# Performance work log

Measured on AMD Instinct MI355X. Metric: run time of the kernel, lower is better.

## Reference

```python
import jax, jax.numpy as jnp
import numpy as np

GRID = 8
S = GRID * GRID          # 64 tokens
D = 256                  # embed dim
H = 4                    # heads
HD = D // H              # 64 head dim
L = 8                    # depth
EPS = 1.1920929e-07      # torch.finfo(float32).eps (nn.RMSNorm eps=None)
RADIUS = 2.5


def _grid_coords():
    y, x = np.meshgrid(np.arange(GRID), np.arange(GRID), indexing='ij')
    return np.stack([y.ravel(), x.ravel()], axis=1).astype(np.float32)  # [S,2]


def _rope_cos_sin():
    coords = _grid_coords()
    dim_half = HD // 2  # 32
    inv_freq = 1.0 / (10000.0 ** (np.arange(0, dim_half, 2, dtype=np.float32) / dim_half))  # [16]
    fy = coords[:, 0:1] * inv_freq[None, :]   # [S,16]
    fx = coords[:, 1:2] * inv_freq[None, :]   # [S,16]
    freqs = np.concatenate([fy, fx], axis=-1)  # [S,32]
    emb = np.concatenate([freqs, freqs], axis=-1)  # [S,64]
    return jnp.asarray(np.cos(emb)), jnp.asarray(np.sin(emb))


def _local_mask():
    coords = _grid_coords()
    d = np.sqrt(((coords[:, None, :] - coords[None, :, :]) ** 2).sum(-1))
    return jnp.asarray(d < RADIUS)  # [S,S] bool


COS, SIN = _rope_cos_sin()
MASK_LOCAL = _local_mask()
MASK_GLOBAL = jnp.ones((S, S), dtype=bool)


def rms(x):
    return x * jax.lax.rsqrt(jnp.mean(x * x, axis=-1, keepdims=True) + EPS)


def householder_Q(vs):
    # vs: [R, HD]; Q = prod of reflections applied as in the torch loop
    def step(Q, v):
        vn = jnp.sum(v * v) + 1e-08
        return Q - (2.0 / vn) * jnp.outer(v, v @ Q), None
    Q, _ = jax.lax.scan(step, jnp.eye(HD, dtype=vs.dtype), vs)
    return Q


def rotate_half(x):
    x1, x2 = jnp.split(x, 2, axis=-1)
    return jnp.concatenate([-x2, x1], axis=-1)


def block(x, vs_l, wqkv, wout, wg, bg, wmg, bmg, wmo, bmo, mask):
    B = x.shape[0]
    xn = rms(x)
    qkv = xn @ wqkv                                # [B,S,3D]
    q, k, v = jnp.split(qkv, 3, axis=-1)
    q = q.reshape(B, S, H, HD).transpose(0, 2, 1, 3)   # [B,H,S,HD]
    k = k.reshape(B, S, H, HD).transpose(0, 2, 1, 3)
    v = v.reshape(B, S, H, HD).transpose(0, 2, 1, 3)
    Q = householder_Q(vs_l)                        # [HD,HD]
    # inverse rotation, standard RoPE, forward rotation
    q = q @ Q.T
    k = k @ Q.T
    cos = COS[None, None]                          # [1,1,S,HD]
    sin = SIN[None, None]
    q = q * cos + rotate_half(q) * sin
    k = k * cos + rotate_half(k) * sin
    q = q @ Q
    k = k @ Q
    scores = jnp.einsum('bhqd,bhkd->bhqk', q, k) / jnp.sqrt(jnp.float32(HD))
    scores = jnp.where(mask[None, None], scores, -jnp.inf)
    attn = jax.nn.softmax(scores, axis=-1)
    out = jnp.einsum('bhqk,bhkd->bhqd', attn, v)   # [B,H,S,HD]
    out = out.transpose(0, 2, 1, 3).reshape(B, S, D)
    out = out @ wout
    gate = jax.nn.sigmoid(out @ wg + bg)
    x = x + out * gate
    xn = rms(x)
    m = xn @ wmg + bmg                             # [B,S,8D]
    g, val = jnp.split(m, 2, axis=-1)
    x = x + (val * jax.nn.gelu(g, approximate=False)) @ wmo + bmo
    return x


def setup_inputs() -> dict:
    key = jax.random.key(0)
    ks = jax.random.split(key, 20)
    B = 1024
    s = 0.02
    return {
        'z_t': jax.random.normal(ks[0], (B, 3, 16, 16), jnp.float32),
        'logsnr': jax.random.normal(ks[1], (B,), jnp.float32),
        'w_patch_in': jax.random.normal(ks[2], (20, D), jnp.float32) * s,
        'b_patch_in': jnp.zeros((D,), jnp.float32),
        'vs': jax.random.normal(ks[3], (L, HD // 2, HD), jnp.float32) * s,
        'w_qkv': jax.random.normal(ks[4], (L, D, 3 * D), jnp.float32) * s,
        'w_out': jax.random.normal(ks[5], (L, D, D), jnp.float32) * s,
        'w_gate': jax.random.normal(ks[6], (L, D, D), jnp.float32) * s,
        'b_gate': jnp.zeros((L, D), jnp.float32),
        'w_mlp_gate': jax.random.normal(ks[7], (L, D, 8 * D), jnp.float32) * s,
        'b_mlp_gate': jnp.zeros((L, 8 * D), jnp.float32),
        'w_mlp_out': jax.random.normal(ks[8], (L, 4 * D, D), jnp.float32) * s,
        'b_mlp_out': jnp.zeros((L, D), jnp.float32),
        'norm_final_w': jnp.ones((D,), jnp.float32),
        'w_head': jax.random.normal(ks[9], (D, D), jnp.float32) * s,
        'b_head': jnp.zeros((D,), jnp.float32),
        'w_patch_out': jax.random.normal(ks[10], (D, 12), jnp.float32) * s,
        'b_patch_out': jnp.zeros((12,), jnp.float32),
    }


def reference(z_t, logsnr, w_patch_in, b_patch_in, vs, w_qkv, w_out, w_gate, b_gate,
              w_mlp_gate, b_mlp_gate, w_mlp_out, b_mlp_out, norm_final_w,
              w_head, b_head, w_patch_out, b_patch_out):
    B = z_t.shape[0]
    # patchify: [B,3,16,16] -> [B,64,12] (2x2 patches over 8x8 grid)
    patches = z_t.reshape(B, 3, GRID, 2, GRID, 2).transpose(0, 2, 4, 1, 3, 5).reshape(B, S, 12)
    # Fourier features of logsnr: num_bands=4, max_range=40
    freqs = (2.0 * np.pi / 40.0) * (2.0 ** jnp.arange(4, dtype=jnp.float32))
    args = logsnr[:, None] * freqs                 # [B,4]
    spins = jnp.concatenate([jnp.sin(args), jnp.cos(args)], axis=-1)  # [B,8]
    spins = jnp.broadcast_to(spins[:, None, :], (B, S, 8))
    x = jnp.concatenate([patches, spins], axis=-1) @ w_patch_in + b_patch_in  # [B,S,D]
    for i in range(L):
        mask = MASK_GLOBAL if (i + 1) % 4 == 0 else MASK_LOCAL
        x = block(x, vs[i], w_qkv[i], w_out[i], w_gate[i], b_gate[i],
                  w_mlp_gate[i], b_mlp_gate[i], w_mlp_out[i], b_mlp_out[i], mask)
    x = rms(x) * norm_final_w
    out = x @ w_head + b_head
    z = out @ w_patch_out + b_patch_out            # [B,S,12]
    z = z.reshape(B, GRID, GRID, 3, 2, 2).transpose(0, 3, 1, 4, 2, 5).reshape(B, 3, 16, 16)
    return z
```

## Files before the change

kernel.cpp:

```cpp
#include <hip/hip_runtime.h>

#define DEV static __device__ __forceinline__

typedef float f32x4 __attribute__((ext_vector_type(4)));
typedef short s16x8 __attribute__((ext_vector_type(8)));
typedef __bf16 bf16x8 __attribute__((ext_vector_type(8)));

DEV unsigned short f2bf(float f) {
  union { float f; unsigned u; } v; v.f = f;
  unsigned r = v.u + 0x7FFFu + ((v.u >> 16) & 1u);
  return (unsigned short)(r >> 16);
}
DEV float bf2f(unsigned short h) {
  union { unsigned u; float f; } v; v.u = ((unsigned)h) << 16;
  return v.f;
}
DEV void g2l16(const void* g, void* l) {
  __builtin_amdgcn_global_load_lds((const __attribute__((address_space(1))) void*)g,
                                   (__attribute__((address_space(3))) void*)l, 16, 0, 0);
}
DEV f32x4 mfma16(bf16x8 a, bf16x8 b, f32x4 c) {
  return __builtin_amdgcn_mfma_f32_16x16x32_bf16(a, b, c, 0, 0, 0);
}
DEV int xcd_swz(int bid, int nwg) {
  return (bid & 7) * (nwg >> 3) + (bid >> 3);
}
DEV float gelu_t(float g) {
  float y = 0.7978845608028654f * (g + 0.044715f * g * g * g);
  float th = 1.f - 2.f * __builtin_amdgcn_rcpf(1.f + __expf(2.f * y));
  return 0.5f * g * (1.f + th);
}

__global__ void k_house(const float* __restrict__ VS, float* __restrict__ Qg) {
  const int l = blockIdx.x, t = threadIdx.x;
  float Qc[64];
#pragma unroll
  for (int i = 0; i < 64; i++) Qc[i] = (i == t) ? 1.f : 0.f;
  for (int rr = 0; rr < 32; rr++) {
    float vt = VS[(size_t)l * 2048 + rr * 64 + t];
    float vn = vt * vt;
#pragma unroll
    for (int o = 1; o < 64; o <<= 1) vn += __shfl_xor(vn, o, 64);
    float vv[64];
#pragma unroll
    for (int i = 0; i < 64; i++) vv[i] = __shfl(vt, i, 64);
    float w0 = 0.f, w1 = 0.f, w2 = 0.f, w3 = 0.f;
#pragma unroll
    for (int i = 0; i < 64; i += 4) {
      w0 = fmaf(vv[i + 0], Qc[i + 0], w0);
      w1 = fmaf(vv[i + 1], Qc[i + 1], w1);
      w2 = fmaf(vv[i + 2], Qc[i + 2], w2);
      w3 = fmaf(vv[i + 3], Qc[i + 3], w3);
    }
    float c = (2.f / (vn + 1e-8f)) * ((w0 + w1) + (w2 + w3));
#pragma unroll
    for (int i = 0; i < 64; i++) Qc[i] = fmaf(-vv[i], c, Qc[i]);
  }
#pragma unroll
  for (int i = 0; i < 64; i++) Qg[(size_t)l * 4096 + i * 64 + t] = Qc[i];
}

__global__ void k_rope(float* __restrict__ C, float* __restrict__ Sn) {
  int idx = blockIdx.x * 256 + threadIdx.x;
  if (idx >= 4096) return;
  int s = idx >> 6, d = idx & 63;
  int dh = d & 31;
  float coord = (dh < 16) ? (float)(s >> 3) : (float)(s & 7);
  int fi = dh & 15;
  float invf = powf(10000.f, -(float)fi / 16.f);
  float ang = coord * invf;
  C[idx] = cosf(ang);
  Sn[idx] = sinf(ang);
}

__global__ __launch_bounds__(256) void k_fold_qkv(const float* __restrict__ W,
                                                  const float* __restrict__ Qg,
                                                  unsigned short* __restrict__ out) {
  __shared__ float qrows[16 * 64];
  __shared__ float tr[16 * 256];
  const int l = blockIdx.x / 48, ng = blockIdx.x % 48;
  const int n0 = ng * 16, t = threadIdx.x;
  const float* Wl = W + (size_t)l * 256 * 768;
  float res[16];
  if (n0 < 512) {
    int part = n0 >> 8, h = (n0 & 255) >> 6, j0 = n0 & 63;
    for (int i = t; i < 1024; i += 256) {
      int jj = i >> 6, dd = i & 63;
      qrows[i] = Qg[(size_t)l * 4096 + (j0 + jj) * 64 + dd];
    }
    __syncthreads();
    const float* wrow = Wl + (size_t)t * 768 + part * 256 + h * 64;
    float wreg[64];
    for (int d = 0; d < 64; d++) wreg[d] = wrow[d];
    for (int jj = 0; jj < 16; jj++) {
      float a = 0.f;
      for (int d = 0; d < 64; d++) a += wreg[d] * qrows[jj * 64 + d];
      res[jj] = a;
    }
  } else {
    for (int jj = 0; jj < 16; jj++) res[jj] = Wl[(size_t)t * 768 + n0 + jj];
    __syncthreads();
  }
  __syncthreads();
  for (int jj = 0; jj < 16; jj++) tr[jj * 256 + t] = res[jj];
  __syncthreads();
  size_t base = (size_t)l * 196608 + (size_t)(n0 >> 4) * 4096;
  int kb = t >> 3, jn0 = (t & 7) * 2;
  s16x8 w0, w1;
  for (int u = 0; u < 8; u++) w0[u] = (short)f2bf(tr[jn0 * 256 + kb * 8 + u]);
  for (int u = 0; u < 8; u++) w1[u] = (short)f2bf(tr[(jn0 + 1) * 256 + kb * 8 + u]);
  *(s16x8*)(out + base + (size_t)t * 16) = w0;
  *(s16x8*)(out + base + (size_t)t * 16 + 8) = w1;
}

__global__ __launch_bounds__(256) void k_fold_w2(const float* __restrict__ WO,
                                                 const float* __restrict__ WG,
                                                 unsigned short* __restrict__ out) {
  __shared__ float wgs[256 * 16];
  __shared__ float tr[16 * 256];
  const int l = blockIdx.x >> 5, ng = blockIdx.x & 31;
  const int n0 = ng * 16, t = threadIdx.x;
  const float* WOl = WO + (size_t)l * 65536;
  float res[16];
  if (n0 < 256) {
    for (int jj = 0; jj < 16; jj++) res[jj] = WOl[(size_t)t * 256 + n0 + jj];
  } else {
    int c0 = n0 - 256;
    const float* WGl = WG + (size_t)l * 65536;
    for (int i = t; i < 4096; i += 256) {
      int k = i >> 4, c = i & 15;
      wgs[i] = WGl[(size_t)k * 256 + c0 + c];
    }
    __syncthreads();
    float a[16];
    for (int c = 0; c < 16; c++) a[c] = 0.f;
    for (int k = 0; k < 256; k++) {
      float wo = WOl[(size_t)t * 256 + k];
      for (int c = 0; c < 16; c++) a[c] += wo * wgs[k * 16 + c];
    }
    for (int c = 0; c < 16; c++) res[c] = a[c];
  }
  __syncthreads();
  for (int jj = 0; jj < 16; jj++) tr[jj * 256 + t] = res[jj];
  __syncthreads();
  size_t base = (size_t)l * 131072 + (size_t)(n0 >> 4) * 4096;
  int kb = t >> 3, jn0 = (t & 7) * 2;
  s16x8 w0, w1;
  for (int u = 0; u < 8; u++) w0[u] = (short)f2bf(tr[jn0 * 256 + kb * 8 + u]);
  for (int u = 0; u < 8; u++) w1[u] = (short)f2bf(tr[(jn0 + 1) * 256 + kb * 8 + u]);
  *(s16x8*)(out + base + (size_t)t * 16) = w0;
  *(s16x8*)(out + base + (size_t)t * 16 + 8) = w1;
}

__global__ __launch_bounds__(256) void k_conv_wmg(const float* __restrict__ W,
                                                  unsigned short* __restrict__ out) {
  __shared__ float tr[16 * 256];
  const int l = blockIdx.x >> 7, ng = blockIdx.x & 127;
  const int n0 = ng * 16, t = threadIdx.x;
  const float* src = W + (size_t)l * 256 * 2048 + (size_t)t * 2048 + n0;
  for (int j = 0; j < 16; j++) tr[j * 256 + t] = src[j];
  __syncthreads();
  size_t base = (size_t)l * 524288 + (size_t)ng * 4096;
  int kb = t >> 3, jn0 = (t & 7) * 2;
  s16x8 w0, w1;
  for (int u = 0; u < 8; u++) w0[u] = (short)f2bf(tr[jn0 * 256 + kb * 8 + u]);
  for (int u = 0; u < 8; u++) w1[u] = (short)f2bf(tr[(jn0 + 1) * 256 + kb * 8 + u]);
  *(s16x8*)(out + base + (size_t)t * 16) = w0;
  *(s16x8*)(out + base + (size_t)t * 16 + 8) = w1;
}

__global__ __launch_bounds__(256) void k_conv_wmo(const float* __restrict__ W,
                                                  unsigned short* __restrict__ out) {
  __shared__ float tr[16 * 256];
  const int l = blockIdx.x >> 4, ng = blockIdx.x & 15;
  const int n0 = ng * 16, t = threadIdx.x;
  const float* Wl = W + (size_t)l * 1024 * 256;
  size_t base = (size_t)l * 262144 + (size_t)ng * 16384;
  for (int c4 = 0; c4 < 4; c4++) {
    int k0 = c4 * 256;
    for (int j = 0; j < 16; j++) tr[j * 256 + t] = Wl[(size_t)(k0 + t) * 256 + n0 + j];
    __syncthreads();
    int kb = t >> 3, jn0 = (t & 7) * 2;
    s16x8 w0, w1;
    for (int u = 0; u < 8; u++) w0[u] = (short)f2bf(tr[jn0 * 256 + kb * 8 + u]);
    for (int u = 0; u < 8; u++) w1[u] = (short)f2bf(tr[(jn0 + 1) * 256 + kb * 8 + u]);
    *(s16x8*)(out + base + (size_t)(k0 >> 3) * 128 + (size_t)t * 16) = w0;
    *(s16x8*)(out + base + (size_t)(k0 >> 3) * 128 + (size_t)t * 16 + 8) = w1;
    __syncthreads();
  }
}

__global__ __launch_bounds__(256) void k_fold_head(const float* __restrict__ WH,
                                                   const float* __restrict__ BH,
                                                   const float* __restrict__ WPO,
                                                   const float* __restrict__ BPO,
                                                   float* __restrict__ WHP,
                                                   float* __restrict__ BHP) {
  __shared__ float wpos[256 * 12];
  const int t = threadIdx.x;
  for (int i = t; i < 3072; i += 256) wpos[i] = WPO[i];
  __syncthreads();
  float a[12];
  for (int c = 0; c < 12; c++) a[c] = 0.f;
  const float* whrow = WH + (size_t)t * 256;
  for (int k = 0; k < 256; k++) {
    float w = whrow[k];
    for (int c = 0; c < 12; c++) a[c] += w * wpos[k * 12 + c];
  }
  for (int c = 0; c < 12; c++) WHP[t * 12 + c] = a[c];
  if (t < 12) {
    float b = BPO[t];
    for (int k = 0; k < 256; k++) b += BH[k] * wpos[k * 12 + t];
    BHP[t] = b;
  }
}

__global__ __launch_bounds__(256) void k_embed(const float* __restrict__ ZT,
                                               const float* __restrict__ LOGSNR,
                                               const float* __restrict__ WPI,
                                               const float* __restrict__ BPI,
                                               float* __restrict__ X) {
  __shared__ float zb[768];
  __shared__ float sp[8];
  const int b = blockIdx.x, t = threadIdx.x;
  for (int i = t; i < 768; i += 256) zb[i] = ZT[(size_t)b * 768 + i];
  if (t < 8) {
    float freq = 0.15707963267948966f * (float)(1 << (t & 3));
    float a = LOGSNR[b] * freq;
    sp[t] = (t < 4) ? sinf(a) : cosf(a);
  }
  __syncthreads();
  float wc[20];
  for (int j = 0; j < 20; j++) wc[j] = WPI[j * 256 + t];
  float bk = BPI[t];
  for (int s = 0; s < 64; s++) {
    int gy = s >> 3, gx = s & 7;
    float acc = bk;
    for (int j = 0; j < 12; j++) {
      int cch = j >> 2, py = (j >> 1) & 1, px = j & 1;
      acc += zb[cch * 256 + (gy * 2 + py) * 16 + gx * 2 + px] * wc[j];
    }
    for (int j = 0; j < 8; j++) acc += sp[j] * wc[12 + j];
    X[((size_t)b * 64 + s) * 256 + t] = acc;
  }
}

__global__ __launch_bounds__(256) void k_rms(const float* __restrict__ X,
                                             unsigned short* __restrict__ XN) {
  const int m0 = blockIdx.x * 16, t = threadIdx.x;
  const int r = t >> 4, cj = t & 15;
  const float* row = X + (size_t)(m0 + r) * 256 + cj * 16;
  float4 a = *(const float4*)(row);
  float4 b = *(const float4*)(row + 4);
  float4 c = *(const float4*)(row + 8);
  float4 d = *(const float4*)(row + 12);
  float ss = a.x * a.x + a.y * a.y + a.z * a.z + a.w * a.w +
             b.x * b.x + b.y * b.y + b.z * b.z + b.w * b.w +
             c.x * c.x + c.y * c.y + c.z * c.z + c.w * c.w +
             d.x * d.x + d.y * d.y + d.z * d.z + d.w * d.w;
  for (int o = 1; o < 16; o <<= 1) ss += __shfl_xor(ss, o, 64);
  float rq = rsqrtf(ss * (1.f / 256.f) + 1.1920929e-07f);
  s16x8 v0, v1;
  v0[0] = (short)f2bf(a.x * rq); v0[1] = (short)f2bf(a.y * rq);
  v0[2] = (short)f2bf(a.z * rq); v0[3] = (short)f2bf(a.w * rq);
  v0[4] = (short)f2bf(b.x * rq); v0[5] = (short)f2bf(b.y * rq);
  v0[6] = (short)f2bf(b.z * rq); v0[7] = (short)f2bf(b.w * rq);
  v1[0] = (short)f2bf(c.x * rq); v1[1] = (short)f2bf(c.y * rq);
  v1[2] = (short)f2bf(c.z * rq); v1[3] = (short)f2bf(c.w * rq);
  v1[4] = (short)f2bf(d.x * rq); v1[5] = (short)f2bf(d.y * rq);
  v1[6] = (short)f2bf(d.z * rq); v1[7] = (short)f2bf(d.w * rq);
  size_t base = ((size_t)blockIdx.x * 32 + cj * 2) * 128 + r * 8;
  *(s16x8*)(XN + base) = v0;
  *(s16x8*)(XN + base + 128) = v1;
}

template <int KD, int NT, int MODE>
__global__ __launch_bounds__(256) void k_gemm_single(const unsigned short* __restrict__ A,
                                                     const unsigned short* __restrict__ Bw,
                                                     unsigned short* __restrict__ Cout,
                                                     const float* __restrict__ bias,
                                                     float* __restrict__ X) {
  __shared__ unsigned short sm[17408];
  unsigned short* la = sm;
  unsigned short* lb = sm + 4096;
  const int t = threadIdx.x;
  const int lane = t & 63, wv = t >> 6;
  const int swz = xcd_swz(blockIdx.x, gridDim.x);
  const int bm = swz / NT, bn = swz % NT;
  const int m0 = bm * 128, n0 = bn * 128;
  const int wm = wv >> 1, wn = wv & 1;
  constexpr int KB8 = KD >> 3;

  f32x4 acc[4][4];
  f32x4 zz = {0.f, 0.f, 0.f, 0.f};
  for (int i = 0; i < 4; i++)
    for (int j = 0; j < 4; j++) acc[i][j] = zz;

  for (int k0 = 0; k0 < KD; k0 += 32) {
    const int kb0 = k0 >> 3;
    for (int ii = 0; ii < 2; ii++) {
      size_t mg = (size_t)(m0 >> 4) + ii * 4 + wv;
      g2l16(A + (mg * KB8 + kb0) * 128 + lane * 8, la + (ii * 4 + wv) * 512 + lane * 8);
    }
    for (int ii = 0; ii < 2; ii++) {
      size_t ng = (size_t)(n0 >> 4) + ii * 4 + wv;
      g2l16(Bw + (ng * KB8 + kb0) * 128 + lane * 8, lb + (ii * 4 + wv) * 512 + lane * 8);
    }
    __syncthreads();
    bf16x8 af[4], bb[4];
    for (int i = 0; i < 4; i++) af[i] = *(const bf16x8*)(la + (wm * 4 + i) * 512 + lane * 8);
    for (int j = 0; j < 4; j++) bb[j] = *(const bf16x8*)(lb + (wn * 4 + j) * 512 + lane * 8);
    for (int i = 0; i < 4; i++)
      for (int j = 0; j < 4; j++) acc[i][j] = mfma16(af[i], bb[j], acc[i][j]);
    __syncthreads();
  }

  const int lr = lane & 15, lg = lane >> 4;
  if constexpr (MODE == 0) {
    unsigned short* lc = sm;
    for (int i = 0; i < 4; i++)
      for (int j = 0; j < 4; j++)
        for (int e = 0; e < 4; e++) {
          int r = wm * 64 + i * 16 + lg * 4 + e;
          int c = wn * 64 + j * 16 + lr;
          lc[r * 136 + c] = f2bf(acc[i][j][e]);
        }
    __syncthreads();
    for (int p = 0; p < 8; p++) {
      int r = p * 16 + (t >> 4);
      int c = (t & 15) * 8;
      *(s16x8*)(Cout + (size_t)(m0 + r) * (NT * 128) + n0 + c) = *(const s16x8*)(lc + r * 136 + c);
    }
  } else {
    float* lcf = (float*)sm;
    for (int p = 0; p < 2; p++) {
      if (wm == p) {
        for (int i = 0; i < 4; i++)
          for (int j = 0; j < 4; j++) {
            int c = wn * 64 + j * 16 + lr;
            float bv = bias[n0 + c];
            for (int e = 0; e < 4; e++) {
              int rr = i * 16 + lg * 4 + e;
              lcf[rr * 132 + c] = acc[i][j][e] + bv;
            }
          }
      }
      __syncthreads();
      for (int k = 0; k < 8; k++) {
        int q = t + 256 * k;
        int row = q >> 5, col4 = q & 31;
        float* xp = X + (size_t)(m0 + p * 64 + row) * 256 + n0 + col4 * 4;
        float4 xv = *(float4*)xp;
        const float* lp = lcf + row * 132 + col4 * 4;
        xv.x += lp[0]; xv.y += lp[1]; xv.z += lp[2]; xv.w += lp[3];
        *(float4*)xp = xv;
      }
      __syncthreads();
    }
  }
}

template <int KD, int MODE>
__global__ __launch_bounds__(256) void k_gemm_dual(const unsigned short* __restrict__ A,
                                                   const unsigned short* __restrict__ B0,
                                                   const unsigned short* __restrict__ B1,
                                                   const float* __restrict__ bias,
                                                   float* __restrict__ X,
                                                   unsigned short* __restrict__ Hout,
                                                   int NT) {
  constexpr int SMSH = (MODE == 0) ? 17408 : 16384;
  __shared__ unsigned short sm[SMSH];
  unsigned short* la = sm;
  unsigned short* lb0 = sm + 8192;
  unsigned short* lb1 = sm + 12288;
  const int t = threadIdx.x, lane = t & 63, wv = t >> 6;
  const int swz = xcd_swz(blockIdx.x, gridDim.x);
  const int bm = swz / NT, bn = swz % NT;
  const int m0 = bm * 128, n0 = bn * 64;
  constexpr int KB8 = KD >> 3;
  f32x4 acc0[2][4], acc1[2][4];
  f32x4 zz = {0.f, 0.f, 0.f, 0.f};
  for (int i = 0; i < 2; i++)
    for (int j = 0; j < 4; j++) { acc0[i][j] = zz; acc1[i][j] = zz; }

  for (int k0 = 0; k0 < KD; k0 += 64) {
    const int kb0 = k0 >> 3;
#pragma unroll
    for (int ii = 0; ii < 4; ii++) {
      int task = ii * 4 + wv;
      int mg = task >> 1, g = task & 1;
      g2l16(A + ((size_t)((m0 >> 4) + mg) * KB8 + kb0 + g * 4) * 128 + lane * 8,
            la + task * 512 + lane * 8);
    }
#pragma unroll
    for (int ii = 0; ii < 2; ii++) {
      int task = ii * 4 + wv;
      int ng = task >> 1, g = task & 1;
      size_t srcoff = ((size_t)((n0 >> 4) + ng) * KB8 + kb0 + g * 4) * 128 + lane * 8;
      g2l16(B0 + srcoff, lb0 + task * 512 + lane * 8);
      g2l16(B1 + srcoff, lb1 + task * 512 + lane * 8);
    }
    __syncthreads();
#pragma unroll
    for (int kk = 0; kk < 2; kk++) {
      bf16x8 af[2];
#pragma unroll
      for (int i = 0; i < 2; i++)
        af[i] = *(const bf16x8*)(la + ((wv * 2 + i) * 8 + kk * 4) * 128 + lane * 8);
#pragma unroll
      for (int j = 0; j < 4; j++) {
        bf16x8 b0 = *(const bf16x8*)(lb0 + (j * 8 + kk * 4) * 128 + lane * 8);
        bf16x8 b1 = *(const bf16x8*)(lb1 + (j * 8 + kk * 4) * 128 + lane * 8);
#pragma unroll
        for (int i = 0; i < 2; i++) {
          acc0[i][j] = mfma16(af[i], b0, acc0[i][j]);
          acc1[i][j] = mfma16(af[i], b1, acc1[i][j]);
        }
      }
    }
    __syncthreads();
  }

  const int lr = lane & 15, lg = lane >> 4;
  if constexpr (MODE == 0) {
    float* lcf = (float*)sm;
    for (int i = 0; i < 2; i++)
      for (int j = 0; j < 4; j++) {
        int c = j * 16 + lr;
        float bv = bias[n0 + c];
        for (int e = 0; e < 4; e++) {
          int r = wv * 32 + i * 16 + lg * 4 + e;
          float o = acc0[i][j][e];
          float g = acc1[i][j][e] + bv;
          lcf[r * 68 + c] = o * __builtin_amdgcn_rcpf(1.f + __expf(-g));
        }
      }
    __syncthreads();
    for (int k = 0; k < 8; k++) {
      int q = t + 256 * k;
      int row = q >> 4, col4 = q & 15;
      float* xp = X + (size_t)(m0 + row) * 256 + n0 + col4 * 4;
      float4 xv = *(float4*)xp;
      const float* lp = lcf + row * 68 + col4 * 4;
      xv.x += lp[0]; xv.y += lp[1]; xv.z += lp[2]; xv.w += lp[3];
      *(float4*)xp = xv;
    }
  } else {
    unsigned short* lc = sm;
    for (int i = 0; i < 2; i++)
      for (int j = 0; j < 4; j++) {
        int cl = j * 16 + lr;
        float bg_ = bias[n0 + cl];
        float bv_ = bias[1024 + n0 + cl];
        for (int e = 0; e < 4; e++) {
          int rl = wv * 32 + i * 16 + lg * 4 + e;
          float g = acc0[i][j][e] + bg_;
          float vv = acc1[i][j][e] + bv_;
          lc[rl * 72 + cl] = f2bf(vv * gelu_t(g));
        }
      }
    __syncthreads();
    for (int it = 0; it < 4; it++) {
      int idx = it * 2048 + t * 8;
      int mg_l = idx >> 10, rem = idx & 1023;
      int kb_l = rem >> 7, r = (rem >> 3) & 15;
      *(s16x8*)(Hout + ((size_t)((m0 >> 4) + mg_l) * 128 + (n0 >> 3) + kb_l) * 128 + r * 8) =
          *(const s16x8*)(lc + (mg_l * 16 + r) * 72 + kb_l * 8);
    }
  }
}

__global__ __launch_bounds__(256) void k_attn(const unsigned short* __restrict__ QKV,
                                              const float* __restrict__ CT,
                                              const float* __restrict__ ST,
                                              unsigned short* __restrict__ AO,
                                              int use_local) {
  __shared__ unsigned short sm[16384];
  unsigned short* qs = sm;
  unsigned short* ks = sm + 4096;
  unsigned short* vt = sm + 8192;
  unsigned short* ps = sm + 12288;
  const int blk = blockIdx.x;
  const int b = blk >> 2, h = blk & 3;
  const int t = threadIdx.x, lane = t & 63, wv = t >> 6;
  const size_t rowbase = (size_t)b * 64 * 768;

  {
    int s = t >> 2, dq = (t & 3) * 8;
    const unsigned short* qrow = QKV + rowbase + (size_t)s * 768 + h * 64;
    s16x8 qlo = *(const s16x8*)(qrow + dq);
    s16x8 qhi = *(const s16x8*)(qrow + dq + 32);
    s16x8 klo = *(const s16x8*)(qrow + 256 + dq);
    s16x8 khi = *(const s16x8*)(qrow + 256 + dq + 32);
    s16x8 oql, oqh, okl, okh;
    for (int e = 0; e < 8; e++) {
      float cl = CT[s * 64 + dq + e], sl = ST[s * 64 + dq + e];
      float ch = CT[s * 64 + dq + 32 + e], sh = ST[s * 64 + dq + 32 + e];
      float ql = bf2f((unsigned short)qlo[e]), qh = bf2f((unsigned short)qhi[e]);
      oql[e] = (short)f2bf((ql * cl - qh * sl) * 0.125f);
      oqh[e] = (short)f2bf((qh * ch + ql * sh) * 0.125f);
      float kl = bf2f((unsigned short)klo[e]), kh = bf2f((unsigned short)khi[e]);
      okl[e] = (short)f2bf(kl * cl - kh * sl);
      okh[e] = (short)f2bf(kh * ch + kl * sh);
    }
    int off_lo = (((s >> 4) * 8 + (dq >> 3)) * 16 + (s & 15)) * 8;
    int off_hi = (((s >> 4) * 8 + (dq >> 3) + 4) * 16 + (s & 15)) * 8;
    *(s16x8*)(qs + off_lo) = oql;
    *(s16x8*)(qs + off_hi) = oqh;
    *(s16x8*)(ks + off_lo) = okl;
    *(s16x8*)(ks + off_hi) = okh;
    int d0 = (t & 3) * 16;
    s16x8 v0 = *(const s16x8*)(qrow + 512 + d0);
    s16x8 v1 = *(const s16x8*)(qrow + 512 + d0 + 8);
    for (int e = 0; e < 8; e++) {
      int d = d0 + e;
      vt[(((d >> 4) * 8 + (s >> 3)) * 16 + (d & 15)) * 8 + (s & 7)] = (unsigned short)v0[e];
      d = d0 + 8 + e;
      vt[(((d >> 4) * 8 + (s >> 3)) * 16 + (d & 15)) * 8 + (s & 7)] = (unsigned short)v1[e];
    }
  }
  __syncthreads();

  f32x4 sc[4];
  f32x4 zz = {0.f, 0.f, 0.f, 0.f};
  for (int j = 0; j < 4; j++) sc[j] = zz;
  for (int kk = 0; kk < 2; kk++) {
    bf16x8 aq = *(const bf16x8*)(qs + wv * 1024 + kk * 512 + lane * 8);
    for (int j = 0; j < 4; j++)
      sc[j] = mfma16(aq, *(const bf16x8*)(ks + j * 1024 + kk * 512 + lane * 8), sc[j]);
  }

  const int lr = lane & 15, lg = lane >> 4;
  for (int e = 0; e < 4; e++) {
    int sq = wv * 16 + lg * 4 + e;
    int yq = sq >> 3, xq = sq & 7;
    float mx = -1e30f;
    float vals[4];
    for (int j = 0; j < 4; j++) {
      int sk = j * 16 + lr;
      float v = sc[j][e];
      if (use_local) {
        int dy = yq - (sk >> 3), dx = xq - (sk & 7);
        if (dy * dy + dx * dx > 6) v = -1e30f;
      }
      vals[j] = v;
      mx = fmaxf(mx, v);
    }
    for (int o = 1; o < 16; o <<= 1) mx = fmaxf(mx, __shfl_xor(mx, o, 64));
    float sum = 0.f;
    for (int j = 0; j < 4; j++) {
      float p = __expf(vals[j] - mx);
      vals[j] = p;
      sum += p;
    }
    for (int o = 1; o < 16; o <<= 1) sum += __shfl_xor(sum, o, 64);
    float inv = __builtin_amdgcn_rcpf(sum);
    for (int j = 0; j < 4; j++) {
      int sk = j * 16 + lr;
      ps[((wv * 8 + (sk >> 3)) * 16 + (sq & 15)) * 8 + (sk & 7)] = f2bf(vals[j] * inv);
    }
  }
  __syncthreads();

  f32x4 oa[4];
  for (int j = 0; j < 4; j++) oa[j] = zz;
  for (int kk = 0; kk < 2; kk++) {
    bf16x8 ap = *(const bf16x8*)(ps + wv * 1024 + kk * 512 + lane * 8);
    for (int j = 0; j < 4; j++)
      oa[j] = mfma16(ap, *(const bf16x8*)(vt + j * 1024 + kk * 512 + lane * 8), oa[j]);
  }
  unsigned short* os = qs + wv * 1024;
  for (int j = 0; j < 4; j++)
    for (int e = 0; e < 4; e++) os[(lg * 4 + e) * 64 + j * 16 + lr] = f2bf(oa[j][e]);
  __syncthreads();
  const size_t obase = ((size_t)(b * 4 + wv) * 32 + h * 8) * 128;
  for (int c = 0; c < 2; c++) {
    int idx = c * 64 + lane;
    int kb = idx >> 4, r = idx & 15;
    *(s16x8*)(AO + obase + (size_t)kb * 128 + r * 8) = *(const s16x8*)(os + r * 64 + kb * 8);
  }
}

__global__ __launch_bounds__(256) void k_head(const float* __restrict__ X,
                                              const float* __restrict__ NW,
                                              const float* __restrict__ WHP,
                                              const float* __restrict__ BHP,
                                              float* __restrict__ OUT) {
  __shared__ float wh[256 * 12];
  __shared__ float nw[256];
  __shared__ float bh[12];
  const int b = blockIdx.x, t = threadIdx.x;
  for (int i = t; i < 3072; i += 256) wh[i] = WHP[i];
  nw[t] = NW[t];
  if (t < 12) bh[t] = BHP[t];
  __syncthreads();
  const int r = t >> 2, qd = t & 3;
  const float* row = X + ((size_t)b * 64 + r) * 256 + qd * 64;
  float ss = 0.f;
  for (int i = 0; i < 64; i++) ss += row[i] * row[i];
  ss += __shfl_xor(ss, 1, 64);
  ss += __shfl_xor(ss, 2, 64);
  float rq = rsqrtf(ss * (1.f / 256.f) + 1.1920929e-07f);
  float accs[12];
  for (int c = 0; c < 12; c++) accs[c] = 0.f;
  for (int i = 0; i < 64; i++) {
    float xf = row[i] * rq * nw[qd * 64 + i];
    const float* wr = wh + (qd * 64 + i) * 12;
    for (int c = 0; c < 12; c++) accs[c] += xf * wr[c];
  }
  for (int c = 0; c < 12; c++) {
    accs[c] += __shfl_xor(accs[c], 1, 64);
    accs[c] += __shfl_xor(accs[c], 2, 64);
  }
  int gy = r >> 3, gx = r & 7;
  for (int u = 0; u < 3; u++) {
    int c = qd * 3 + u;
    float val = accs[c] + bh[c];
    int ch = c >> 2, py = (c >> 1) & 1, px = c & 1;
    OUT[(size_t)b * 768 + ch * 256 + (gy * 2 + py) * 16 + (gx * 2 + px)] = val;
  }
}

extern "C" void kernel_launch(void* const* d_in, const int* in_sizes, int n_in,
                              void* d_out, int out_size, void* d_ws, size_t ws_size,
                              hipStream_t stream) {
  (void)n_in; (void)out_size; (void)ws_size;
  const float* z_t    = (const float*)d_in[0];
  const float* logsnr = (const float*)d_in[1];
  const float* wpi    = (const float*)d_in[2];
  const float* bpi    = (const float*)d_in[3];
  const float* vs     = (const float*)d_in[4];
  const float* wqkv   = (const float*)d_in[5];
  const float* wout   = (const float*)d_in[6];
  const float* wgate  = (const float*)d_in[7];
  const float* bgate  = (const float*)d_in[8];
  const float* wmg    = (const float*)d_in[9];
  const float* bmg    = (const float*)d_in[10];
  const float* wmo    = (const float*)d_in[11];
  const float* bmo    = (const float*)d_in[12];
  const float* nfw    = (const float*)d_in[13];
  const float* whead  = (const float*)d_in[14];
  const float* bhead  = (const float*)d_in[15];
  const float* wpo    = (const float*)d_in[16];
  const float* bpo    = (const float*)d_in[17];
  float* OUT = (float*)d_out;

  const int Bn = in_sizes[0] / 768;
  const int Mtot = Bn * 64;

  char* w = (char*)d_ws;
  auto alloc = [&](size_t bytes) {
    char* p = w;
    w += (bytes + 255) & ~(size_t)255;
    return p;
  };
  float* Qg  = (float*)alloc((size_t)8 * 4096 * 4);
  float* Ct  = (float*)alloc(4096 * 4);
  float* St  = (float*)alloc(4096 * 4);
  float* WHP = (float*)alloc(3072 * 4);
  float* BHP = (float*)alloc(64);
  unsigned short* WqkvS = (unsigned short*)alloc((size_t)8 * 768 * 256 * 2);
  unsigned short* W2S   = (unsigned short*)alloc((size_t)8 * 512 * 256 * 2);
  unsigned short* WmgS  = (unsigned short*)alloc((size_t)8 * 2048 * 256 * 2);
  unsigned short* WmoS  = (unsigned short*)alloc((size_t)8 * 256 * 1024 * 2);
  float* X = (float*)alloc((size_t)Mtot * 256 * 4);
  unsigned short* XN  = (unsigned short*)alloc((size_t)Mtot * 256 * 2);
  unsigned short* BIG = (unsigned short*)alloc((size_t)Mtot * 1024 * 2);
  unsigned short* QKVb = BIG;
  unsigned short* AOb  = BIG + (size_t)Mtot * 768;
  unsigned short* Hb   = BIG;

  k_house<<<8, 64, 0, stream>>>(vs, Qg);
  k_rope<<<16, 256, 0, stream>>>(Ct, St);
  k_fold_qkv<<<8 * 48, 256, 0, stream>>>(wqkv, Qg, WqkvS);
  k_fold_w2<<<8 * 32, 256, 0, stream>>>(wout, wgate, W2S);
  k_conv_wmg<<<8 * 128, 256, 0, stream>>>(wmg, WmgS);
  k_conv_wmo<<<8 * 16, 256, 0, stream>>>(wmo, WmoS);
  k_fold_head<<<1, 256, 0, stream>>>(whead, bhead, wpo, bpo, WHP, BHP);
  k_embed<<<Bn, 256, 0, stream>>>(z_t, logsnr, wpi, bpi, X);

  for (int l = 0; l < 8; l++) {
    k_rms<<<Mtot / 16, 256, 0, stream>>>(X, XN);
    k_gemm_single<256, 6, 0><<<(Mtot / 128) * 6, 256, 0, stream>>>(
        XN, WqkvS + (size_t)l * 196608, QKVb, nullptr, nullptr);
    k_attn<<<Bn * 4, 256, 0, stream>>>(QKVb, Ct, St, AOb, ((l + 1) % 4) ? 1 : 0);
    k_gemm_dual<256, 0><<<(Mtot / 128) * 4, 256, 0, stream>>>(
        AOb, W2S + (size_t)l * 131072, W2S + (size_t)l * 131072 + 65536,
        bgate + l * 256, X, nullptr, 4);
    k_rms<<<Mtot / 16, 256, 0, stream>>>(X, XN);
    k_gemm_dual<256, 1><<<(Mtot / 128) * 16, 256, 0, stream>>>(
        XN, WmgS + (size_t)l * 524288, WmgS + (size_t)l * 524288 + 262144,
        bmg + l * 2048, nullptr, Hb, 16);
    k_gemm_single<1024, 2, 1><<<(Mtot / 128) * 2, 256, 0, stream>>>(
        Hb, WmoS + (size_t)l * 262144, nullptr, bmo + l * 256, X);
  }
  k_head<<<Bn, 256, 0, stream>>>(X, nfw, WHP, BHP, OUT);
}
```

Measured before the change: 2.832 ms.

## Fuse MLP-out GEMM residual add with next layer's RMSNorm

```diff
diff --git a/kernel.cpp b/kernel.cpp
--- a/kernel.cpp
+++ b/kernel.cpp
@@ -316,47 +316,19 @@
   }
 
   const int lr = lane & 15, lg = lane >> 4;
-  if constexpr (MODE == 0) {
-    unsigned short* lc = sm;
-    for (int i = 0; i < 4; i++)
-      for (int j = 0; j < 4; j++)
-        for (int e = 0; e < 4; e++) {
-          int r = wm * 64 + i * 16 + lg * 4 + e;
-          int c = wn * 64 + j * 16 + lr;
-          lc[r * 136 + c] = f2bf(acc[i][j][e]);
-        }
-    __syncthreads();
-    for (int p = 0; p < 8; p++) {
-      int r = p * 16 + (t >> 4);
-      int c = (t & 15) * 8;
-      *(s16x8*)(Cout + (size_t)(m0 + r) * (NT * 128) + n0 + c) = *(const s16x8*)(lc + r * 136 + c);
-    }
-  } else {
-    float* lcf = (float*)sm;
-    for (int p = 0; p < 2; p++) {
-      if (wm == p) {
-        for (int i = 0; i < 4; i++)
-          for (int j = 0; j < 4; j++) {
-            int c = wn * 64 + j * 16 + lr;
-            float bv = bias[n0 + c];
-            for (int e = 0; e < 4; e++) {
-              int rr = i * 16 + lg * 4 + e;
-              lcf[rr * 132 + c] = acc[i][j][e] + bv;
-            }
-          }
+  unsigned short* lc = sm;
+  for (int i = 0; i < 4; i++)
+    for (int j = 0; j < 4; j++)
+      for (int e = 0; e < 4; e++) {
+        int r = wm * 64 + i * 16 + lg * 4 + e;
+        int c = wn * 64 + j * 16 + lr;
+        lc[r * 136 + c] = f2bf(acc[i][j][e]);
       }
-      __syncthreads();
-      for (int k = 0; k < 8; k++) {
-        int q = t + 256 * k;
-        int row = q >> 5, col4 = q & 31;
-        float* xp = X + (size_t)(m0 + p * 64 + row) * 256 + n0 + col4 * 4;
-        float4 xv = *(float4*)xp;
-        const float* lp = lcf + row * 132 + col4 * 4;
-        xv.x += lp[0]; xv.y += lp[1]; xv.z += lp[2]; xv.w += lp[3];
-        *(float4*)xp = xv;
-      }
-      __syncthreads();
-    }
+  __syncthreads();
+  for (int p = 0; p < 8; p++) {
+    int r = p * 16 + (t >> 4);
+    int c = (t & 15) * 8;
+    *(s16x8*)(Cout + (size_t)(m0 + r) * (NT * 128) + n0 + c) = *(const s16x8*)(lc + r * 136 + c);
   }
 }
 
@@ -467,6 +439,113 @@
       *(s16x8*)(Hout + ((size_t)((m0 >> 4) + mg_l) * 128 + (n0 >> 3) + kb_l) * 128 + r * 8) =
           *(const s16x8*)(lc + (mg_l * 16 + r) * 72 + kb_l * 8);
     }
+  }
+}
+
+__global__ __launch_bounds__(256) void k_mlpout_rms(const unsigned short* __restrict__ A,
+                                                    const unsigned short* __restrict__ Bw,
+                                                    const float* __restrict__ bias,
+                                                    float* __restrict__ X,
+                                                    unsigned short* __restrict__ XN) {
+  __shared__ unsigned short sm[11008];
+  unsigned short* la = sm;
+  unsigned short* lb = sm + 2048;
+  float* ssqw = (float*)(sm + 10240);
+  float* rqb = ssqw + 320;
+  const int t = threadIdx.x, lane = t & 63, wv = t >> 6;
+  const int bm = xcd_swz(blockIdx.x, gridDim.x);
+  const int m0 = bm * 64;
+  const int lr = lane & 15, lg = lane >> 4;
+
+  f32x4 acc[4][4];
+  f32x4 zz = {0.f, 0.f, 0.f, 0.f};
+#pragma unroll
+  for (int i = 0; i < 4; i++)
+#pragma unroll
+    for (int j = 0; j < 4; j++) acc[i][j] = zz;
+
+  for (int k0 = 0; k0 < 1024; k0 += 32) {
+    const int kb0 = k0 >> 3;
+#pragma unroll
+    for (int ii = 0; ii < 5; ii++) {
+      int tt = ii * 4 + wv;
+      if (tt < 4) {
+        g2l16(A + ((size_t)((m0 >> 4) + tt) * 128 + kb0) * 128 + lane * 8,
+              la + tt * 512 + lane * 8);
+      } else {
+        int ng = tt - 4;
+        g2l16(Bw + ((size_t)ng * 128 + kb0) * 128 + lane * 8,
+              lb + ng * 512 + lane * 8);
+      }
+    }
+    __syncthreads();
+    bf16x8 af[4], bb[4];
+#pragma unroll
+    for (int i = 0; i < 4; i++) af[i] = *(const bf16x8*)(la + i * 512 + lane * 8);
+#pragma unroll
+    for (int j = 0; j < 4; j++) bb[j] = *(const bf16x8*)(lb + (wv * 4 + j) * 512 + lane * 8);
+#pragma unroll
+    for (int i = 0; i < 4; i++)
+#pragma unroll
+      for (int j = 0; j < 4; j++) acc[i][j] = mfma16(af[i], bb[j], acc[i][j]);
+    __syncthreads();
+  }
+
+  float ssqp[16];
+#pragma unroll
+  for (int q = 0; q < 16; q++) ssqp[q] = 0.f;
+#pragma unroll
+  for (int i = 0; i < 4; i++)
+#pragma unroll
+    for (int j = 0; j < 4; j++) {
+      int c = wv * 64 + j * 16 + lr;
+      float bv = bias[c];
+#pragma unroll
+      for (int e = 0; e < 4; e++) {
+        int r = m0 + i * 16 + lg * 4 + e;
+        float xv = X[(size_t)r * 256 + c] + acc[i][j][e] + bv;
+        X[(size_t)r * 256 + c] = xv;
+        ssqp[i * 4 + e] += xv * xv;
+      }
+    }
+#pragma unroll
+  for (int q = 0; q < 16; q++) {
+    float s = ssqp[q];
+    s += __shfl_xor(s, 1, 64);
+    s += __shfl_xor(s, 2, 64);
+    s += __shfl_xor(s, 4, 64);
+    s += __shfl_xor(s, 8, 64);
+    ssqp[q] = s;
+  }
+  if (lr == 0) {
+#pragma unroll
+    for (int i = 0; i < 4; i++)
+#pragma unroll
+      for (int e = 0; e < 4; e++) ssqw[(i * 16 + lg * 4 + e) * 5 + wv] = ssqp[i * 4 + e];
+  }
+  __syncthreads();
+  if (t < 64) {
+    float s = ssqw[t * 5] + ssqw[t * 5 + 1] + ssqw[t * 5 + 2] + ssqw[t * 5 + 3];
+    rqb[t] = rsqrtf(s * (1.f / 256.f) + 1.1920929e-07f);
+  }
+  __syncthreads();
+
+#pragma unroll
+  for (int it = 0; it < 8; it++) {
+    int rc = it >> 1, half = it & 1;
+    int r15 = t & 15, ccl = t >> 4;
+    int cc = half * 16 + ccl;
+    int row_l = rc * 16 + r15;
+    const float* xp = X + (size_t)(m0 + row_l) * 256 + cc * 8;
+    float4 x0 = *(const float4*)xp;
+    float4 x1 = *(const float4*)(xp + 4);
+    float rqv = rqb[row_l];
+    s16x8 o;
+    o[0] = (short)f2bf(x0.x * rqv); o[1] = (short)f2bf(x0.y * rqv);
+    o[2] = (short)f2bf(x0.z * rqv); o[3] = (short)f2bf(x0.w * rqv);
+    o[4] = (short)f2bf(x1.x * rqv); o[5] = (short)f2bf(x1.y * rqv);
+    o[6] = (short)f2bf(x1.z * rqv); o[7] = (short)f2bf(x1.w * rqv);
+    *(s16x8*)(XN + ((size_t)((m0 >> 4) + rc) * 32 + cc) * 128 + r15 * 8) = o;
   }
 }
 
@@ -678,9 +757,9 @@
   k_conv_wmo<<<8 * 16, 256, 0, stream>>>(wmo, WmoS);
   k_fold_head<<<1, 256, 0, stream>>>(whead, bhead, wpo, bpo, WHP, BHP);
   k_embed<<<Bn, 256, 0, stream>>>(z_t, logsnr, wpi, bpi, X);
+  k_rms<<<Mtot / 16, 256, 0, stream>>>(X, XN);
 
   for (int l = 0; l < 8; l++) {
-    k_rms<<<Mtot / 16, 256, 0, stream>>>(X, XN);
     k_gemm_single<256, 6, 0><<<(Mtot / 128) * 6, 256, 0, stream>>>(
         XN, WqkvS + (size_t)l * 196608, QKVb, nullptr, nullptr);
     k_attn<<<Bn * 4, 256, 0, stream>>>(QKVb, Ct, St, AOb, ((l + 1) % 4) ? 1 : 0);
@@ -691,8 +770,8 @@
     k_gemm_dual<256, 1><<<(Mtot / 128) * 16, 256, 0, stream>>>(
         XN, WmgS + (size_t)l * 524288, WmgS + (size_t)l * 524288 + 262144,
         bmg + l * 2048, nullptr, Hb, 16);
-    k_gemm_single<1024, 2, 1><<<(Mtot / 128) * 2, 256, 0, stream>>>(
-        Hb, WmoS + (size_t)l * 262144, nullptr, bmo + l * 256, X);
+    k_mlpout_rms<<<Mtot / 64, 256, 0, stream>>>(
+        Hb, WmoS + (size_t)l * 262144, bmo + l * 256, X, XN);
   }
   k_head<<<Bn, 256, 0, stream>>>(X, nfw, WHP, BHP, OUT);
 }
```

After: 2.733 ms. 1.04x faster.
